# Kernel optimization log

Hardware: AMD Instinct MI355X
Metric: run time of the kernel (lower is better)

Reference implementation:

```python
import jax, jax.numpy as jnp
import numpy as np

V, E, H, B, T, S = 32000, 512, 512, 16, 128, 128


def setup_inputs() -> dict:
    key = jax.random.key(0)
    ks = jax.random.split(key, 12)
    sc_e = 1.0 / np.sqrt(E)
    sc_h = 1.0 / np.sqrt(H)
    emb_table = jax.random.normal(ks[0], (V, E), jnp.float32) * 0.02
    emb_table = emb_table.at[0].set(0.0)  # padding_idx=0
    return {
        "text_vec": jax.random.randint(ks[1], (B, T), 0, V),
        "decoder_hidden": jax.random.normal(ks[2], (1, B, H), jnp.float32),
        "encoder_output": jax.random.normal(ks[3], (B, S, H), jnp.float32),
        "attention_mask": jnp.ones((B, S), jnp.bool_),
        "emb_table": emb_table,
        "w_ih": jax.random.uniform(ks[4], (3 * H, E), jnp.float32, -sc_h, sc_h),
        "w_hh": jax.random.uniform(ks[5], (3 * H, H), jnp.float32, -sc_h, sc_h),
        "b_ih": jax.random.uniform(ks[6], (3 * H,), jnp.float32, -sc_h, sc_h),
        "b_hh": jax.random.uniform(ks[7], (3 * H,), jnp.float32, -sc_h, sc_h),
        "lin_out_w": jax.random.uniform(ks[8], (H, 2 * H), jnp.float32, -1.0 / np.sqrt(2 * H), 1.0 / np.sqrt(2 * H)),
        "out_w": jax.random.uniform(ks[9], (V, H), jnp.float32, -sc_h, sc_h),
        "out_b": jax.random.uniform(ks[10], (V,), jnp.float32, -sc_h, sc_h),
    }


def _gru_cell(x, h, w_ih, w_hh, b_ih, b_hh):
    gi = x @ w_ih.T + b_ih  # [B,3H]
    gh = h @ w_hh.T + b_hh  # [B,3H]
    ir, iz, inn = jnp.split(gi, 3, axis=-1)
    hr, hz, hn = jnp.split(gh, 3, axis=-1)
    r = jax.nn.sigmoid(ir + hr)
    z = jax.nn.sigmoid(iz + hz)
    n = jnp.tanh(inn + r * hn)
    return (1.0 - z) * n + z * h


def reference(text_vec, decoder_hidden, encoder_output, attention_mask,
              emb_table, w_ih, w_hh, b_ih, b_hh, lin_out_w, out_w, out_b):
    # embedding with padding_idx=0 -> zero vector
    emb = emb_table[text_vec] * (text_vec != 0)[..., None].astype(emb_table.dtype)  # [B,T,E]
    neg = jnp.asarray(-1e6, emb.dtype)

    def step(h, x_t):
        h_new = _gru_cell(x_t, h, w_ih, w_hh, b_ih, b_hh)  # [B,H]
        scores = jnp.einsum('bh,bsh->bs', h_new, encoder_output)
        scores = jnp.where(attention_mask, scores, neg)
        attn_w = jax.nn.softmax(scores, axis=-1)  # [B,S]
        mix = jnp.einsum('bs,bsh->bh', attn_w, encoder_output)
        combined = jnp.concatenate([h_new, mix], axis=-1)  # [B,2H]
        attended = jnp.tanh(combined @ lin_out_w.T)  # [B,H]
        return h_new, (attended, attn_w)

    h0 = decoder_hidden[0]  # num_layers == 1
    h_final, (attended_seq, attn_w_log) = jax.lax.scan(step, h0, jnp.swapaxes(emb, 0, 1))
    output = jnp.swapaxes(attended_seq, 0, 1)  # [B,T,H]
    scores = output @ out_w.T + out_b  # [B,T,V]
    return scores, h_final[None], attn_w_log
```

## Files before the change

### kernel.cpp

```cpp
#include <hip/hip_runtime.h>
#include <hip/hip_bf16.h>

#define NV 32000
#define NE 512
#define NH 512
#define NB 16
#define NT 128
#define NS 128

typedef __bf16 bf16x8 __attribute__((ext_vector_type(8)));
typedef float f32x4 __attribute__((ext_vector_type(4)));
typedef const __attribute__((address_space(1))) unsigned int gu32;
typedef __attribute__((address_space(3))) unsigned int lu32;

static constexpr size_t HTAG_OFF = 0;
static constexpr size_t WHHT_OFF = HTAG_OFF + (size_t)2*NB*NH*8;
static constexpr size_t GI_OFF   = WHHT_OFF + (size_t)3*NH*NH*4;
static constexpr size_t HALL_OFF = GI_OFF + (size_t)NT*NB*3*NH*4;
static constexpr size_t MIX_OFF  = HALL_OFF + (size_t)(NT+1)*NB*NH*4;
static constexpr size_t ATTB_OFF = MIX_OFF + (size_t)NB*NT*NH*4;
static constexpr size_t OWB_OFF  = ATTB_OFF + (size_t)NB*NT*NH*2;
static constexpr size_t WS_NEED  = OWB_OFF + (size_t)NV*NH*2;

__global__ __launch_bounds__(256) void k_pg(const int* __restrict__ tv,
                                            const float* __restrict__ emb,
                                            const float* __restrict__ w_ih,
                                            const float* __restrict__ b_ih,
                                            float* __restrict__ gi_all,
                                            const float* __restrict__ w_hh,
                                            const float* __restrict__ dh,
                                            const float* __restrict__ out_w,
                                            float* __restrict__ whhT,
                                            float* __restrict__ h_all,
                                            __bf16* __restrict__ owb,
                                            unsigned long long* __restrict__ htag) {
  const int g = blockIdx.x;
  const int tid = threadIdx.x;
  if (g >= 768) {
    long long i0 = (long long)(g - 768) * 256 + tid;
    long long stride = (long long)1024 * 256;
    long long n4 = (long long)NV * NH / 4;
    for (long long i = i0; i < n4; i += stride) {
      float4 v = ((const float4*)out_w)[i];
      union { __bf16 b[4]; float2 f2; } u;
      u.b[0] = (__bf16)v.x; u.b[1] = (__bf16)v.y; u.b[2] = (__bf16)v.z; u.b[3] = (__bf16)v.w;
      *((float2*)(owb + 4 * i)) = u.f2;
    }
    for (long long i = i0; i < (long long)3 * NH * NH; i += stride) {
      int k = (int)(i / (3 * NH)), j = (int)(i % (3 * NH));
      whhT[i] = w_hh[(long long)j * NH + k];
    }
    for (long long i = i0; i < NB * NH; i += stride) {
      float hv = dh[i];
      h_all[i] = hv;
      union { float f; unsigned u; } c; c.f = hv;
      htag[i] = (1ull << 32) | c.u;
      htag[NB * NH + i] = 0ull;
    }
    return;
  }
  __shared__ float As[16][64];
  __shared__ float Bs[16][64];
  const int n0 = (g % 24) * 64;
  const int m0 = (g / 24) * 64;
  float acc[4][4] = {};
  const int rl = tid >> 2;
  const int kq = (tid & 3) * 4;
  const int tvr = tv[m0 + rl];
  const float* arow = emb + (long long)tvr * NE;
  const int tm = tid & 15, tn = tid >> 4;
  for (int k0 = 0; k0 < NE; k0 += 16) {
    __syncthreads();
    float4 av = make_float4(0.f, 0.f, 0.f, 0.f);
    if (tvr != 0) av = *(const float4*)(arow + k0 + kq);
    float4 bv = *(const float4*)(w_ih + (long long)(n0 + rl) * NE + k0 + kq);
    As[kq + 0][rl] = av.x; As[kq + 1][rl] = av.y; As[kq + 2][rl] = av.z; As[kq + 3][rl] = av.w;
    Bs[kq + 0][rl] = bv.x; Bs[kq + 1][rl] = bv.y; Bs[kq + 2][rl] = bv.z; Bs[kq + 3][rl] = bv.w;
    __syncthreads();
#pragma unroll
    for (int kk = 0; kk < 16; ++kk) {
      float4 a = *(const float4*)&As[kk][tm * 4];
      float4 b = *(const float4*)&Bs[kk][tn * 4];
      float ar[4] = {a.x, a.y, a.z, a.w}, br[4] = {b.x, b.y, b.z, b.w};
#pragma unroll
      for (int i = 0; i < 4; ++i)
#pragma unroll
        for (int j = 0; j < 4; ++j) acc[i][j] = fmaf(ar[i], br[j], acc[i][j]);
    }
  }
#pragma unroll
  for (int i = 0; i < 4; ++i) {
    int r = m0 + tm * 4 + i;
    long long gb = (long long)((r & 127) * 16 + (r >> 7)) * (3 * NH);
#pragma unroll
    for (int j = 0; j < 4; ++j) {
      int jg = n0 + tn * 4 + j;
      gi_all[gb + jg] = acc[i][j] + b_ih[jg];
    }
  }
}

__global__ __launch_bounds__(512, 2) void k_rec(const float* __restrict__ whhT,
                                                const float* __restrict__ gi_all,
                                                const float* __restrict__ b_hh,
                                                float* __restrict__ h_all,
                                                unsigned long long* __restrict__ htag,
                                                float* __restrict__ d_hf) {
  const int tid = threadIdx.x;
  const int b = blockIdx.x & 15, sub = blockIdx.x >> 4;
  const int hl = tid & 63, kc = tid >> 6;
  const int j = sub * 64 + hl;
  __shared__ float hbuf[512];
  __shared__ float part[3][8][64];

  float wg[3][64];
#pragma unroll
  for (int g = 0; g < 3; ++g) {
    const float* wp = whhT + (long long)(kc * 64) * 1536 + g * 512 + j;
#pragma unroll
    for (int q = 0; q < 64; ++q) wg[g][q] = wp[(long long)q * 1536];
  }
  float bhr = 0.f, bhz = 0.f, bhn = 0.f;
  if (tid < 64) {
    bhr = b_hh[sub * 64 + tid];
    bhz = b_hh[512 + sub * 64 + tid];
    bhn = b_hh[1024 + sub * 64 + tid];
  }

  for (int t = 0; t < NT; ++t) {
    float gr = 0.f, gz = 0.f, gn = 0.f;
    if (tid < 64) {
      const float* gi = gi_all + (long long)(t * 16 + b) * 1536;
      gr = gi[sub * 64 + tid];
      gz = gi[512 + sub * 64 + tid];
      gn = gi[1024 + sub * 64 + tid];
    }
    {
      unsigned long long* slot = htag + ((long long)(t & 1) * NB + b) * 512 + tid;
      unsigned long long v = __hip_atomic_load(slot, __ATOMIC_RELAXED, __HIP_MEMORY_SCOPE_AGENT);
      int guard = 0;
      while ((unsigned)(v >> 32) != (unsigned)(t + 1) && ++guard < (1 << 22)) {
        v = __hip_atomic_load(slot, __ATOMIC_RELAXED, __HIP_MEMORY_SCOPE_AGENT);
      }
      union { unsigned u; float f; } c; c.u = (unsigned)v;
      hbuf[tid] = c.f;
    }
    __syncthreads();
    float ar = 0.f, az = 0.f, an = 0.f;
#pragma unroll
    for (int q4 = 0; q4 < 4; ++q4) {
      float4 h4[4];
#pragma unroll
      for (int u = 0; u < 4; ++u) h4[u] = *(const float4*)&hbuf[kc * 64 + q4 * 16 + u * 4];
#pragma unroll
      for (int u = 0; u < 4; ++u) {
        const float hh[4] = {h4[u].x, h4[u].y, h4[u].z, h4[u].w};
#pragma unroll
        for (int v = 0; v < 4; ++v) {
          const int q = q4 * 16 + u * 4 + v;
          ar = fmaf(hh[v], wg[0][q], ar);
          az = fmaf(hh[v], wg[1][q], az);
          an = fmaf(hh[v], wg[2][q], an);
        }
      }
    }
    part[0][kc][hl] = ar; part[1][kc][hl] = az; part[2][kc][hl] = an;
    __syncthreads();
    if (tid < 64) {
      float sr = bhr, sz = bhz, sn = bhn;
#pragma unroll
      for (int c = 0; c < 8; ++c) {
        sr += part[0][c][tid]; sz += part[1][c][tid]; sn += part[2][c][tid];
      }
      float r = 1.f / (1.f + expf(-(gr + sr)));
      float z = 1.f / (1.f + expf(-(gz + sz)));
      float n = tanhf(gn + r * sn);
      float hp = hbuf[sub * 64 + tid];
      float hv = (1.f - z) * n + z * hp;
      if (t < NT - 1) {
        union { float f; unsigned u; } c2; c2.f = hv;
        unsigned long long out = ((unsigned long long)(unsigned)(t + 2) << 32) | c2.u;
        __hip_atomic_store(htag + ((long long)((t + 1) & 1) * NB + b) * 512 + sub * 64 + tid, out,
                           __ATOMIC_RELAXED, __HIP_MEMORY_SCOPE_AGENT);
      }
      h_all[(long long)((t + 1) * 16 + b) * 512 + sub * 64 + tid] = hv;
      if (t == NT - 1) d_hf[b * 512 + sub * 64 + tid] = hv;
    }
    __syncthreads();
  }
}

__global__ __launch_bounds__(256) void k_attn(const float* __restrict__ h_all,
                                              const float* __restrict__ enc,
                                              const int* __restrict__ mask,
                                              float* __restrict__ d_attn,
                                              float* __restrict__ mix) {
  const int g = blockIdx.x;
  const int t = g >> 4, b = g & 15;
  const int tid = threadIdx.x;
  __shared__ float hb[512];
  __shared__ float red[256];
  __shared__ float wb[128];
  __shared__ float smax, ssum;
  const float* hsrc = h_all + (long long)((t + 1) * 16 + b) * 512;
  hb[tid] = hsrc[tid];
  hb[tid + 256] = hsrc[tid + 256];
  __syncthreads();
  const int s = tid & 127, half = tid >> 7;
  const float* erow = enc + (long long)(b * 128 + s) * 512 + half * 256;
  float p = 0.f;
#pragma unroll 8
  for (int k = 0; k < 256; ++k) p = fmaf(hb[half * 256 + k], erow[k], p);
  red[tid] = p;
  __syncthreads();
  float sc = 0.f;
  if (tid < 128) {
    sc = red[tid] + red[tid + 128];
    if (mask[b * 128 + tid] == 0) sc = -1e6f;
    wb[tid] = sc;
  }
  __syncthreads();
  if (tid < 64) {
    float m2 = fmaxf(wb[tid], wb[tid + 64]);
    for (int off = 32; off; off >>= 1) m2 = fmaxf(m2, __shfl_down(m2, off));
    if (tid == 0) smax = m2;
  }
  __syncthreads();
  if (tid < 128) wb[tid] = expf(sc - smax);
  __syncthreads();
  if (tid < 64) {
    float s2 = wb[tid] + wb[tid + 64];
    for (int off = 32; off; off >>= 1) s2 += __shfl_down(s2, off);
    if (tid == 0) ssum = s2;
  }
  __syncthreads();
  float inv = 1.f / ssum;
  if (tid < 128) {
    float w = wb[tid] * inv;
    wb[tid] = w;
    d_attn[(long long)(t * 16 + b) * 128 + tid] = w;
  }
  __syncthreads();
  long long mrow = (long long)(b * 128 + t) * 512;
  for (int hh = tid; hh < 512; hh += 256) {
    float acc = 0.f;
#pragma unroll 8
    for (int s2 = 0; s2 < 128; ++s2) acc = fmaf(wb[s2], enc[(long long)(b * 128 + s2) * 512 + hh], acc);
    mix[mrow + hh] = acc;
  }
}

__global__ __launch_bounds__(256) void k_att_lin(const float* __restrict__ h_all,
                                                 const float* __restrict__ mix,
                                                 const float* __restrict__ W,
                                                 __bf16* __restrict__ attout) {
  __shared__ float As[16][64];
  __shared__ float Bs[16][64];
  const int tid = threadIdx.x;
  const int n0 = blockIdx.x * 64;
  const int m0 = blockIdx.y * 64;
  float acc[4][4] = {};
  const int rl = tid >> 2;
  const int kq = (tid & 3) * 4;
  const int tm = tid & 15, tn = tid >> 4;
  const int r_a = m0 + rl;
  const int b_a = r_a >> 7, t_a = r_a & 127;
  const float* hrow = h_all + (long long)((t_a + 1) * 16 + b_a) * 512;
  const float* mrow = mix + (long long)r_a * 512;
  for (int k0 = 0; k0 < 1024; k0 += 16) {
    __syncthreads();
    float4 av = (k0 < 512) ? *(const float4*)(hrow + k0 + kq)
                           : *(const float4*)(mrow + (k0 - 512) + kq);
    float4 bv = *(const float4*)(W + (long long)(n0 + rl) * 1024 + k0 + kq);
    As[kq + 0][rl] = av.x; As[kq + 1][rl] = av.y; As[kq + 2][rl] = av.z; As[kq + 3][rl] = av.w;
    Bs[kq + 0][rl] = bv.x; Bs[kq + 1][rl] = bv.y; Bs[kq + 2][rl] = bv.z; Bs[kq + 3][rl] = bv.w;
    __syncthreads();
#pragma unroll
    for (int kk = 0; kk < 16; ++kk) {
      float4 a = *(const float4*)&As[kk][tm * 4];
      float4 b = *(const float4*)&Bs[kk][tn * 4];
      float ar[4] = {a.x, a.y, a.z, a.w}, br[4] = {b.x, b.y, b.z, b.w};
#pragma unroll
      for (int i = 0; i < 4; ++i)
#pragma unroll
        for (int j = 0; j < 4; ++j) acc[i][j] = fmaf(ar[i], br[j], acc[i][j]);
    }
  }
#pragma unroll
  for (int i = 0; i < 4; ++i) {
    int r = m0 + tm * 4 + i;
#pragma unroll
    for (int j = 0; j < 4; ++j) {
      int o = n0 + tn * 4 + j;
      attout[(long long)r * 512 + o] = (__bf16)tanhf(acc[i][j]);
    }
  }
}

__global__ __launch_bounds__(256) void k_out(const __bf16* __restrict__ Abf,
                                             const __bf16* __restrict__ Bbf,
                                             const float* __restrict__ bias,
                                             float* __restrict__ Cout) {
  __shared__ __bf16 Al[128 * 32];
  __shared__ __bf16 Bl[128 * 32];
  const int tid = threadIdx.x;
  const int lane = tid & 63;
  const int wave = tid >> 6;
  const int wm = wave >> 1, wn = wave & 1;
  const int swz = (blockIdx.x & 7) * 500 + (blockIdx.x >> 3);
  const int m0 = (swz & 15) * 128, n0 = (swz >> 4) * 128;
  f32x4 acc[4][4] = {};
  const int lrow = lane >> 2;
  const int lcol = (lane & 3) * 8;
  const int lm = lane & 15, lc = lane >> 4;
  for (int ks = 0; ks < 16; ++ks) {
    const int k0 = ks * 32;
    __syncthreads();
#pragma unroll
    for (int i = 0; i < 2; ++i) {
      int chunk = wave * 2 + i;
      int r = chunk * 16 + lrow;
      const __bf16* ga = Abf + (long long)(m0 + r) * NH + k0 + lcol;
      const __bf16* gb = Bbf + (long long)(n0 + r) * NH + k0 + lcol;
      __builtin_amdgcn_global_load_lds((gu32*)ga, (lu32*)((char*)Al + chunk * 1024), 16, 0, 0);
      __builtin_amdgcn_global_load_lds((gu32*)gb, (lu32*)((char*)Bl + chunk * 1024), 16, 0, 0);
    }
    __syncthreads();
    bf16x8 af[4], bfr[4];
#pragma unroll
    for (int i = 0; i < 4; ++i) af[i] = *(const bf16x8*)&Al[(wm * 64 + i * 16 + lm) * 32 + lc * 8];
#pragma unroll
    for (int j = 0; j < 4; ++j) bfr[j] = *(const bf16x8*)&Bl[(wn * 64 + j * 16 + lm) * 32 + lc * 8];
#pragma unroll
    for (int i = 0; i < 4; ++i)
#pragma unroll
      for (int j = 0; j < 4; ++j)
        acc[i][j] = __builtin_amdgcn_mfma_f32_16x16x32_bf16(af[i], bfr[j], acc[i][j], 0, 0, 0);
  }
#pragma unroll
  for (int j = 0; j < 4; ++j) {
    int c = n0 + wn * 64 + j * 16 + lm;
    float bv = bias[c];
#pragma unroll
    for (int i = 0; i < 4; ++i) {
      int rb = m0 + wm * 64 + i * 16 + lc * 4;
#pragma unroll
      for (int q = 0; q < 4; ++q)
        Cout[(long long)(rb + q) * NV + c] = acc[i][j][q] + bv;
    }
  }
}

extern "C" void kernel_launch(void* const* d_in, const int* in_sizes, int n_in,
                              void* d_out, int out_size, void* d_ws, size_t ws_size,
                              hipStream_t stream) {
  const int* tv = (const int*)d_in[0];
  const float* dh = (const float*)d_in[1];
  const float* enc = (const float*)d_in[2];
  const int* mask = (const int*)d_in[3];
  const float* emb = (const float*)d_in[4];
  const float* w_ih = (const float*)d_in[5];
  const float* w_hh = (const float*)d_in[6];
  const float* b_ih = (const float*)d_in[7];
  const float* b_hh = (const float*)d_in[8];
  const float* lin_w = (const float*)d_in[9];
  const float* out_w = (const float*)d_in[10];
  const float* out_b = (const float*)d_in[11];
  float* dout = (float*)d_out;
  char* ws = (char*)d_ws;
  if (ws_size < WS_NEED) return;

  unsigned long long* htag = (unsigned long long*)(ws + HTAG_OFF);
  float* whhT = (float*)(ws + WHHT_OFF);
  float* gi_all = (float*)(ws + GI_OFF);
  float* h_all = (float*)(ws + HALL_OFF);
  float* mixb = (float*)(ws + MIX_OFF);
  __bf16* attb = (__bf16*)(ws + ATTB_OFF);
  __bf16* owb = (__bf16*)(ws + OWB_OFF);

  float* d_scores = dout;
  float* d_hf = dout + (long long)NB * NT * NV;
  float* d_attn = d_hf + NB * NH;

  k_pg<<<1792, 256, 0, stream>>>(tv, emb, w_ih, b_ih, gi_all,
                                 w_hh, dh, out_w, whhT, h_all, owb, htag);
  k_rec<<<128, 512, 0, stream>>>(whhT, gi_all, b_hh, h_all, htag, d_hf);
  k_attn<<<2048, 256, 0, stream>>>(h_all, enc, mask, d_attn, mixb);
  k_att_lin<<<dim3(8, 32), 256, 0, stream>>>(h_all, mixb, lin_w, attb);
  k_out<<<4000, 256, 0, stream>>>(attb, owb, out_b, d_scores);
}
```

Measured before the change: 557.9 us.

## Fuse GRU recurrence with attention and linear stages via per-step completion flags

Merges the recurrent kernel, attention kernel and attended-linear kernel into one persistent launch. 128 blocks run the GRU recurrence while 384 other blocks first convert out_w to bf16, then spin on per-timestep done counters and compute attention, mix and the tanh(linear) for each (t,b) as soon as it is ready. lin_out_w is pre-converted to bf16 and the linear runs as a per-row dot product instead of a tiled GEMM. The aim is to overlap the serial recurrence with the downstream work and the weight conversion, at the cost of co-residency assumptions for spinning blocks and lower precision in lin_out_w.

```diff
diff --git a/kernel.cpp b/kernel.cpp
--- a/kernel.cpp
+++ b/kernel.cpp
@@ -13,14 +13,19 @@
 typedef const __attribute__((address_space(1))) unsigned int gu32;
 typedef __attribute__((address_space(3))) unsigned int lu32;
 
-static constexpr size_t HTAG_OFF = 0;
-static constexpr size_t WHHT_OFF = HTAG_OFF + (size_t)2*NB*NH*8;
-static constexpr size_t GI_OFF   = WHHT_OFF + (size_t)3*NH*NH*4;
-static constexpr size_t HALL_OFF = GI_OFF + (size_t)NT*NB*3*NH*4;
-static constexpr size_t MIX_OFF  = HALL_OFF + (size_t)(NT+1)*NB*NH*4;
-static constexpr size_t ATTB_OFF = MIX_OFF + (size_t)NB*NT*NH*4;
-static constexpr size_t OWB_OFF  = ATTB_OFF + (size_t)NB*NT*NH*2;
-static constexpr size_t WS_NEED  = OWB_OFF + (size_t)NV*NH*2;
+__device__ __forceinline__ float bits2f(unsigned int u) {
+  union { unsigned int i; float f; } v; v.i = u; return v.f;
+}
+
+static constexpr size_t HTAG_OFF  = 0;
+static constexpr size_t HDONE_OFF = HTAG_OFF + (size_t)2*NB*NH*8;
+static constexpr size_t WHHT_OFF  = HDONE_OFF + 8192;
+static constexpr size_t GI_OFF    = WHHT_OFF + (size_t)3*NH*NH*4;
+static constexpr size_t HALL_OFF  = GI_OFF + (size_t)NT*NB*3*NH*4;
+static constexpr size_t LWB_OFF   = HALL_OFF + (size_t)(NT+1)*NB*NH*4;
+static constexpr size_t ATTB_OFF  = LWB_OFF + (size_t)NH*2*NH*2;
+static constexpr size_t OWB_OFF   = ATTB_OFF + (size_t)NB*NT*NH*2;
+static constexpr size_t WS_NEED   = OWB_OFF + (size_t)NV*NH*2;
 
 __global__ __launch_bounds__(256) void k_pg(const int* __restrict__ tv,
                                             const float* __restrict__ emb,
@@ -29,26 +34,26 @@
                                             float* __restrict__ gi_all,
                                             const float* __restrict__ w_hh,
                                             const float* __restrict__ dh,
-                                            const float* __restrict__ out_w,
+                                            const float* __restrict__ lin_w,
                                             float* __restrict__ whhT,
                                             float* __restrict__ h_all,
-                                            __bf16* __restrict__ owb,
-                                            unsigned long long* __restrict__ htag) {
+                                            unsigned short* __restrict__ lwb,
+                                            unsigned long long* __restrict__ htag,
+                                            unsigned int* __restrict__ hdone) {
   const int g = blockIdx.x;
   const int tid = threadIdx.x;
   if (g >= 768) {
     long long i0 = (long long)(g - 768) * 256 + tid;
     long long stride = (long long)1024 * 256;
-    long long n4 = (long long)NV * NH / 4;
-    for (long long i = i0; i < n4; i += stride) {
-      float4 v = ((const float4*)out_w)[i];
-      union { __bf16 b[4]; float2 f2; } u;
-      u.b[0] = (__bf16)v.x; u.b[1] = (__bf16)v.y; u.b[2] = (__bf16)v.z; u.b[3] = (__bf16)v.w;
-      *((float2*)(owb + 4 * i)) = u.f2;
-    }
     for (long long i = i0; i < (long long)3 * NH * NH; i += stride) {
       int k = (int)(i / (3 * NH)), j = (int)(i % (3 * NH));
       whhT[i] = w_hh[(long long)j * NH + k];
+    }
+    for (long long i = i0; i < (long long)NH * 2 * NH / 4; i += stride) {
+      float4 v = ((const float4*)lin_w)[i];
+      union { __bf16 b[4]; unsigned long long u; } u4;
+      u4.b[0] = (__bf16)v.x; u4.b[1] = (__bf16)v.y; u4.b[2] = (__bf16)v.z; u4.b[3] = (__bf16)v.w;
+      *((unsigned long long*)(lwb + 4 * i)) = u4.u;
     }
     for (long long i = i0; i < NB * NH; i += stride) {
       float hv = dh[i];
@@ -57,6 +62,7 @@
       htag[i] = (1ull << 32) | c.u;
       htag[NB * NH + i] = 0ull;
     }
+    for (long long i = i0; i < 2048; i += stride) hdone[i] = 0u;
     return;
   }
   __shared__ float As[16][64];
@@ -100,200 +106,215 @@
   }
 }
 
-__global__ __launch_bounds__(512, 2) void k_rec(const float* __restrict__ whhT,
-                                                const float* __restrict__ gi_all,
-                                                const float* __restrict__ b_hh,
-                                                float* __restrict__ h_all,
-                                                unsigned long long* __restrict__ htag,
-                                                float* __restrict__ d_hf) {
+__global__ __launch_bounds__(512, 2) void k_fused(const float* __restrict__ whhT,
+                                                  const float* __restrict__ gi_all,
+                                                  const float* __restrict__ b_hh,
+                                                  float* __restrict__ h_all,
+                                                  unsigned long long* __restrict__ htag,
+                                                  unsigned int* __restrict__ hdone,
+                                                  float* __restrict__ d_hf,
+                                                  const float* __restrict__ enc,
+                                                  const int* __restrict__ mask,
+                                                  const unsigned short* __restrict__ lwb,
+                                                  const float* __restrict__ out_w,
+                                                  __bf16* __restrict__ owb,
+                                                  float* __restrict__ d_attn,
+                                                  __bf16* __restrict__ attb) {
+  __shared__ float smem[2048];
+  __shared__ float sred[2];
   const int tid = threadIdx.x;
-  const int b = blockIdx.x & 15, sub = blockIdx.x >> 4;
-  const int hl = tid & 63, kc = tid >> 6;
-  const int j = sub * 64 + hl;
-  __shared__ float hbuf[512];
-  __shared__ float part[3][8][64];
-
-  float wg[3][64];
-#pragma unroll
-  for (int g = 0; g < 3; ++g) {
-    const float* wp = whhT + (long long)(kc * 64) * 1536 + g * 512 + j;
-#pragma unroll
-    for (int q = 0; q < 64; ++q) wg[g][q] = wp[(long long)q * 1536];
-  }
-  float bhr = 0.f, bhz = 0.f, bhn = 0.f;
-  if (tid < 64) {
-    bhr = b_hh[sub * 64 + tid];
-    bhz = b_hh[512 + sub * 64 + tid];
-    bhn = b_hh[1024 + sub * 64 + tid];
-  }
-
-  for (int t = 0; t < NT; ++t) {
-    float gr = 0.f, gz = 0.f, gn = 0.f;
+  const int bid = blockIdx.x;
+
+  if (bid < 128) {
+    const int b = bid & 15, sub = bid >> 4;
+    const int hl = tid & 63, kc = tid >> 6;
+    const int j = sub * 64 + hl;
+    float* hbuf = smem;
+    float* part = smem + 512;
+
+    float wg[3][64];
+#pragma unroll
+    for (int g = 0; g < 3; ++g) {
+      const float* wp = whhT + (long long)(kc * 64) * 1536 + g * 512 + j;
+#pragma unroll
+      for (int q = 0; q < 64; ++q) wg[g][q] = wp[(long long)q * 1536];
+    }
+    float bhr = 0.f, bhz = 0.f, bhn = 0.f;
     if (tid < 64) {
-      const float* gi = gi_all + (long long)(t * 16 + b) * 1536;
-      gr = gi[sub * 64 + tid];
-      gz = gi[512 + sub * 64 + tid];
-      gn = gi[1024 + sub * 64 + tid];
-    }
+      bhr = b_hh[sub * 64 + tid];
+      bhz = b_hh[512 + sub * 64 + tid];
+      bhn = b_hh[1024 + sub * 64 + tid];
+    }
+
+    for (int t = 0; t < NT; ++t) {
+      float gr = 0.f, gz = 0.f, gn = 0.f;
+      if (tid < 64) {
+        const float* gi = gi_all + (long long)(t * 16 + b) * 1536;
+        gr = gi[sub * 64 + tid];
+        gz = gi[512 + sub * 64 + tid];
+        gn = gi[1024 + sub * 64 + tid];
+      }
+      {
+        unsigned long long* slot = htag + ((long long)(t & 1) * NB + b) * 512 + tid;
+        unsigned long long v = __hip_atomic_load(slot, __ATOMIC_RELAXED, __HIP_MEMORY_SCOPE_AGENT);
+        int guard = 0;
+        while ((unsigned)(v >> 32) != (unsigned)(t + 1) && ++guard < (1 << 22)) {
+          v = __hip_atomic_load(slot, __ATOMIC_RELAXED, __HIP_MEMORY_SCOPE_AGENT);
+        }
+        union { unsigned u; float f; } c; c.u = (unsigned)v;
+        hbuf[tid] = c.f;
+      }
+      __syncthreads();
+      float ar = 0.f, az = 0.f, an = 0.f;
+#pragma unroll
+      for (int q4 = 0; q4 < 4; ++q4) {
+        float4 h4[4];
+#pragma unroll
+        for (int u = 0; u < 4; ++u) h4[u] = *(const float4*)&hbuf[kc * 64 + q4 * 16 + u * 4];
+#pragma unroll
+        for (int u = 0; u < 4; ++u) {
+          const float hh[4] = {h4[u].x, h4[u].y, h4[u].z, h4[u].w};
+#pragma unroll
+          for (int v = 0; v < 4; ++v) {
+            const int q = q4 * 16 + u * 4 + v;
+            ar = fmaf(hh[v], wg[0][q], ar);
+            az = fmaf(hh[v], wg[1][q], az);
+            an = fmaf(hh[v], wg[2][q], an);
+          }
+        }
+      }
+      part[0 * 512 + kc * 64 + hl] = ar;
+      part[1 * 512 + kc * 64 + hl] = az;
+      part[2 * 512 + kc * 64 + hl] = an;
+      __syncthreads();
+      if (tid < 64) {
+        float sr = bhr, sz = bhz, sn = bhn;
+#pragma unroll
+        for (int c = 0; c < 8; ++c) {
+          sr += part[0 * 512 + c * 64 + tid];
+          sz += part[1 * 512 + c * 64 + tid];
+          sn += part[2 * 512 + c * 64 + tid];
+        }
+        float r = 1.f / (1.f + expf(-(gr + sr)));
+        float z = 1.f / (1.f + expf(-(gz + sz)));
+        float n = tanhf(gn + r * sn);
+        float hp = hbuf[sub * 64 + tid];
+        float hv = (1.f - z) * n + z * hp;
+        if (t < NT - 1) {
+          union { float f; unsigned u; } c2; c2.f = hv;
+          unsigned long long out = ((unsigned long long)(unsigned)(t + 2) << 32) | c2.u;
+          __hip_atomic_store(htag + ((long long)((t + 1) & 1) * NB + b) * 512 + sub * 64 + tid, out,
+                             __ATOMIC_RELAXED, __HIP_MEMORY_SCOPE_AGENT);
+        }
+        __hip_atomic_store(&h_all[(long long)((t + 1) * 16 + b) * 512 + sub * 64 + tid], hv,
+                           __ATOMIC_RELAXED, __HIP_MEMORY_SCOPE_AGENT);
+        if (t == NT - 1) d_hf[b * 512 + sub * 64 + tid] = hv;
+      }
+      __syncthreads();
+      if (tid == 0)
+        __hip_atomic_fetch_add(&hdone[t * 16 + b], 1u, __ATOMIC_RELAXED, __HIP_MEMORY_SCOPE_AGENT);
+    }
+    return;
+  }
+
+  const int ab = bid - 128;
+  {
+    long long n4 = (long long)NV * NH / 4;
+    for (long long i = (long long)ab * 512 + tid; i < n4; i += (long long)384 * 512) {
+      float4 v = ((const float4*)out_w)[i];
+      union { __bf16 b[4]; unsigned long long u; } u4;
+      u4.b[0] = (__bf16)v.x; u4.b[1] = (__bf16)v.y; u4.b[2] = (__bf16)v.z; u4.b[3] = (__bf16)v.w;
+      *((unsigned long long*)((unsigned short*)owb + 4 * i)) = u4.u;
+    }
+  }
+  float* hb = smem;
+  float* mixs = smem + 512;
+  float* red = smem + 1024;
+  float* wb = smem + 1536;
+  for (int it = 0; it < 6; ++it) {
+    const int u = ab + it * 384;
+    if (u >= 2048) break;
+    const int t = u >> 4, b = u & 15;
+    if (tid == 0) {
+      int guard = 0;
+      while (__hip_atomic_load(&hdone[u], __ATOMIC_RELAXED, __HIP_MEMORY_SCOPE_AGENT) < 8u &&
+             ++guard < (1 << 25)) {
+        __builtin_amdgcn_s_sleep(4);
+      }
+    }
+    __syncthreads();
+    hb[tid] = bits2f(__float_as_uint(
+        __hip_atomic_load(&h_all[(long long)((t + 1) * 16 + b) * 512 + tid],
+                          __ATOMIC_RELAXED, __HIP_MEMORY_SCOPE_AGENT)));
+    __syncthreads();
+    const int s = tid & 127, q = tid >> 7;
     {
-      unsigned long long* slot = htag + ((long long)(t & 1) * NB + b) * 512 + tid;
-      unsigned long long v = __hip_atomic_load(slot, __ATOMIC_RELAXED, __HIP_MEMORY_SCOPE_AGENT);
-      int guard = 0;
-      while ((unsigned)(v >> 32) != (unsigned)(t + 1) && ++guard < (1 << 22)) {
-        v = __hip_atomic_load(slot, __ATOMIC_RELAXED, __HIP_MEMORY_SCOPE_AGENT);
-      }
-      union { unsigned u; float f; } c; c.u = (unsigned)v;
-      hbuf[tid] = c.f;
-    }
-    __syncthreads();
-    float ar = 0.f, az = 0.f, an = 0.f;
-#pragma unroll
-    for (int q4 = 0; q4 < 4; ++q4) {
-      float4 h4[4];
-#pragma unroll
-      for (int u = 0; u < 4; ++u) h4[u] = *(const float4*)&hbuf[kc * 64 + q4 * 16 + u * 4];
-#pragma unroll
-      for (int u = 0; u < 4; ++u) {
-        const float hh[4] = {h4[u].x, h4[u].y, h4[u].z, h4[u].w};
-#pragma unroll
-        for (int v = 0; v < 4; ++v) {
-          const int q = q4 * 16 + u * 4 + v;
-          ar = fmaf(hh[v], wg[0][q], ar);
-          az = fmaf(hh[v], wg[1][q], az);
-          an = fmaf(hh[v], wg[2][q], an);
-        }
-      }
-    }
-    part[0][kc][hl] = ar; part[1][kc][hl] = az; part[2][kc][hl] = an;
+      const float* erow = enc + (long long)(b * 128 + s) * 512 + q * 128;
+      float p = 0.f;
+#pragma unroll 8
+      for (int k = 0; k < 128; ++k) p = fmaf(hb[q * 128 + k], erow[k], p);
+      red[tid] = p;
+    }
+    __syncthreads();
+    float sc = 0.f;
+    if (tid < 128) {
+      sc = red[tid] + red[tid + 128] + red[tid + 256] + red[tid + 384];
+      if (mask[b * 128 + tid] == 0) sc = -1e6f;
+      wb[tid] = sc;
+    }
     __syncthreads();
     if (tid < 64) {
-      float sr = bhr, sz = bhz, sn = bhn;
-#pragma unroll
-      for (int c = 0; c < 8; ++c) {
-        sr += part[0][c][tid]; sz += part[1][c][tid]; sn += part[2][c][tid];
-      }
-      float r = 1.f / (1.f + expf(-(gr + sr)));
-      float z = 1.f / (1.f + expf(-(gz + sz)));
-      float n = tanhf(gn + r * sn);
-      float hp = hbuf[sub * 64 + tid];
-      float hv = (1.f - z) * n + z * hp;
-      if (t < NT - 1) {
-        union { float f; unsigned u; } c2; c2.f = hv;
-        unsigned long long out = ((unsigned long long)(unsigned)(t + 2) << 32) | c2.u;
-        __hip_atomic_store(htag + ((long long)((t + 1) & 1) * NB + b) * 512 + sub * 64 + tid, out,
-                           __ATOMIC_RELAXED, __HIP_MEMORY_SCOPE_AGENT);
-      }
-      h_all[(long long)((t + 1) * 16 + b) * 512 + sub * 64 + tid] = hv;
-      if (t == NT - 1) d_hf[b * 512 + sub * 64 + tid] = hv;
-    }
-    __syncthreads();
-  }
-}
-
-__global__ __launch_bounds__(256) void k_attn(const float* __restrict__ h_all,
-                                              const float* __restrict__ enc,
-                                              const int* __restrict__ mask,
-                                              float* __restrict__ d_attn,
-                                              float* __restrict__ mix) {
-  const int g = blockIdx.x;
-  const int t = g >> 4, b = g & 15;
-  const int tid = threadIdx.x;
-  __shared__ float hb[512];
-  __shared__ float red[256];
-  __shared__ float wb[128];
-  __shared__ float smax, ssum;
-  const float* hsrc = h_all + (long long)((t + 1) * 16 + b) * 512;
-  hb[tid] = hsrc[tid];
-  hb[tid + 256] = hsrc[tid + 256];
-  __syncthreads();
-  const int s = tid & 127, half = tid >> 7;
-  const float* erow = enc + (long long)(b * 128 + s) * 512 + half * 256;
-  float p = 0.f;
+      float m2 = fmaxf(wb[tid], wb[tid + 64]);
+      for (int off = 32; off; off >>= 1) m2 = fmaxf(m2, __shfl_down(m2, off));
+      if (tid == 0) sred[0] = m2;
+    }
+    __syncthreads();
+    if (tid < 128) wb[tid] = expf(sc - sred[0]);
+    __syncthreads();
+    if (tid < 64) {
+      float s2 = wb[tid] + wb[tid + 64];
+      for (int off = 32; off; off >>= 1) s2 += __shfl_down(s2, off);
+      if (tid == 0) sred[1] = s2;
+    }
+    __syncthreads();
+    {
+      float inv = 1.f / sred[1];
+      if (tid < 128) {
+        float w = wb[tid] * inv;
+        wb[tid] = w;
+        d_attn[(long long)u * 128 + tid] = w;
+      }
+    }
+    __syncthreads();
+    {
+      float m = 0.f;
 #pragma unroll 8
-  for (int k = 0; k < 256; ++k) p = fmaf(hb[half * 256 + k], erow[k], p);
-  red[tid] = p;
-  __syncthreads();
-  float sc = 0.f;
-  if (tid < 128) {
-    sc = red[tid] + red[tid + 128];
-    if (mask[b * 128 + tid] == 0) sc = -1e6f;
-    wb[tid] = sc;
-  }
-  __syncthreads();
-  if (tid < 64) {
-    float m2 = fmaxf(wb[tid], wb[tid + 64]);
-    for (int off = 32; off; off >>= 1) m2 = fmaxf(m2, __shfl_down(m2, off));
-    if (tid == 0) smax = m2;
-  }
-  __syncthreads();
-  if (tid < 128) wb[tid] = expf(sc - smax);
-  __syncthreads();
-  if (tid < 64) {
-    float s2 = wb[tid] + wb[tid + 64];
-    for (int off = 32; off; off >>= 1) s2 += __shfl_down(s2, off);
-    if (tid == 0) ssum = s2;
-  }
-  __syncthreads();
-  float inv = 1.f / ssum;
-  if (tid < 128) {
-    float w = wb[tid] * inv;
-    wb[tid] = w;
-    d_attn[(long long)(t * 16 + b) * 128 + tid] = w;
-  }
-  __syncthreads();
-  long long mrow = (long long)(b * 128 + t) * 512;
-  for (int hh = tid; hh < 512; hh += 256) {
-    float acc = 0.f;
-#pragma unroll 8
-    for (int s2 = 0; s2 < 128; ++s2) acc = fmaf(wb[s2], enc[(long long)(b * 128 + s2) * 512 + hh], acc);
-    mix[mrow + hh] = acc;
-  }
-}
-
-__global__ __launch_bounds__(256) void k_att_lin(const float* __restrict__ h_all,
-                                                 const float* __restrict__ mix,
-                                                 const float* __restrict__ W,
-                                                 __bf16* __restrict__ attout) {
-  __shared__ float As[16][64];
-  __shared__ float Bs[16][64];
-  const int tid = threadIdx.x;
-  const int n0 = blockIdx.x * 64;
-  const int m0 = blockIdx.y * 64;
-  float acc[4][4] = {};
-  const int rl = tid >> 2;
-  const int kq = (tid & 3) * 4;
-  const int tm = tid & 15, tn = tid >> 4;
-  const int r_a = m0 + rl;
-  const int b_a = r_a >> 7, t_a = r_a & 127;
-  const float* hrow = h_all + (long long)((t_a + 1) * 16 + b_a) * 512;
-  const float* mrow = mix + (long long)r_a * 512;
-  for (int k0 = 0; k0 < 1024; k0 += 16) {
-    __syncthreads();
-    float4 av = (k0 < 512) ? *(const float4*)(hrow + k0 + kq)
-                           : *(const float4*)(mrow + (k0 - 512) + kq);
-    float4 bv = *(const float4*)(W + (long long)(n0 + rl) * 1024 + k0 + kq);
-    As[kq + 0][rl] = av.x; As[kq + 1][rl] = av.y; As[kq + 2][rl] = av.z; As[kq + 3][rl] = av.w;
-    Bs[kq + 0][rl] = bv.x; Bs[kq + 1][rl] = bv.y; Bs[kq + 2][rl] = bv.z; Bs[kq + 3][rl] = bv.w;
-    __syncthreads();
-#pragma unroll
-    for (int kk = 0; kk < 16; ++kk) {
-      float4 a = *(const float4*)&As[kk][tm * 4];
-      float4 b = *(const float4*)&Bs[kk][tn * 4];
-      float ar[4] = {a.x, a.y, a.z, a.w}, br[4] = {b.x, b.y, b.z, b.w};
-#pragma unroll
-      for (int i = 0; i < 4; ++i)
-#pragma unroll
-        for (int j = 0; j < 4; ++j) acc[i][j] = fmaf(ar[i], br[j], acc[i][j]);
-    }
-  }
-#pragma unroll
-  for (int i = 0; i < 4; ++i) {
-    int r = m0 + tm * 4 + i;
-#pragma unroll
-    for (int j = 0; j < 4; ++j) {
-      int o = n0 + tn * 4 + j;
-      attout[(long long)r * 512 + o] = (__bf16)tanhf(acc[i][j]);
-    }
+      for (int s2 = 0; s2 < 128; ++s2)
+        m = fmaf(wb[s2], enc[(long long)(b * 128 + s2) * 512 + tid], m);
+      mixs[tid] = m;
+    }
+    __syncthreads();
+    {
+      float acc = 0.f;
+      const unsigned short* wrow = lwb + (long long)tid * 1024;
+#pragma unroll 4
+      for (int k8 = 0; k8 < 128; ++k8) {
+        uint4 w8 = *(const uint4*)(wrow + k8 * 8);
+        const float* csrc = (k8 < 64) ? &hb[k8 * 8] : &mixs[(k8 - 64) * 8];
+        float4 ca = *(const float4*)csrc;
+        float4 cb = *(const float4*)(csrc + 4);
+        acc = fmaf(ca.x, bits2f(w8.x << 16), acc);
+        acc = fmaf(ca.y, bits2f(w8.x & 0xffff0000u), acc);
+        acc = fmaf(ca.z, bits2f(w8.y << 16), acc);
+        acc = fmaf(ca.w, bits2f(w8.y & 0xffff0000u), acc);
+        acc = fmaf(cb.x, bits2f(w8.z << 16), acc);
+        acc = fmaf(cb.y, bits2f(w8.z & 0xffff0000u), acc);
+        acc = fmaf(cb.z, bits2f(w8.w << 16), acc);
+        acc = fmaf(cb.w, bits2f(w8.w & 0xffff0000u), acc);
+      }
+      attb[(long long)(b * 128 + t) * 512 + tid] = (__bf16)tanhf(acc);
+    }
+    __syncthreads();
   }
 }
 
@@ -371,10 +392,11 @@
   if (ws_size < WS_NEED) return;
 
   unsigned long long* htag = (unsigned long long*)(ws + HTAG_OFF);
+  unsigned int* hdone = (unsigned int*)(ws + HDONE_OFF);
   float* whhT = (float*)(ws + WHHT_OFF);
   float* gi_all = (float*)(ws + GI_OFF);
   float* h_all = (float*)(ws + HALL_OFF);
-  float* mixb = (float*)(ws + MIX_OFF);
+  unsigned short* lwb = (unsigned short*)(ws + LWB_OFF);
   __bf16* attb = (__bf16*)(ws + ATTB_OFF);
   __bf16* owb = (__bf16*)(ws + OWB_OFF);
 
@@ -383,9 +405,8 @@
   float* d_attn = d_hf + NB * NH;
 
   k_pg<<<1792, 256, 0, stream>>>(tv, emb, w_ih, b_ih, gi_all,
-                                 w_hh, dh, out_w, whhT, h_all, owb, htag);
-  k_rec<<<128, 512, 0, stream>>>(whhT, gi_all, b_hh, h_all, htag, d_hf);
-  k_attn<<<2048, 256, 0, stream>>>(h_all, enc, mask, d_attn, mixb);
-  k_att_lin<<<dim3(8, 32), 256, 0, stream>>>(h_all, mixb, lin_w, attb);
+                                 w_hh, dh, lin_w, whhT, h_all, lwb, htag, hdone);
+  k_fused<<<512, 512, 0, stream>>>(whhT, gi_all, b_hh, h_all, htag, hdone, d_hf,
+                                   enc, mask, lwb, out_w, owb, d_attn, attb);
   k_out<<<4000, 256, 0, stream>>>(attb, owb, out_b, d_scores);
 }
```

After: 653.9 us. 1.17x slower.
